# Performance work log

Measured on AMD Instinct MI355X. Metric: run time of the kernel, lower is better.

The kernel has to match this reference:

```python
import jax, jax.numpy as jnp
import numpy as np

DEGREE = 64
LEN_H = 2
INIT_H = 4.0
FEATURES = [256, 512, 512, 256]
BATCH = 1024


def _frozen_kh():
    # get_frozen_para: k = arange(-floor(d/2), ceil(d/2)+1); h = 1/(init_h*(1+arange(len_h))) (inverse decay)
    k = jnp.arange(-np.floor(DEGREE / 2), np.ceil(DEGREE / 2) + 1, dtype=jnp.float32)  # (degree+1,)
    h = 1.0 / (INIT_H * (1.0 + jnp.arange(LEN_H, dtype=jnp.float32)))  # (len_h,)
    return k, h


def setup_inputs() -> dict:
    key = jax.random.key(0)
    ks = jax.random.split(key, 7)
    inp = {"x": jax.random.normal(ks[0], (BATCH, FEATURES[0]), dtype=jnp.float32)}
    i = 1
    for li, (fi, fo) in enumerate(zip(FEATURES[:-1], FEATURES[1:])):
        # initialization='None': plain normal coeffs (matches source)
        inp[f"coeffs{li}"] = jax.random.normal(ks[i], (fi, fo, LEN_H, DEGREE + 1), dtype=jnp.float32)
        inp[f"alpha{li}"] = jax.random.normal(ks[i + 1], (fi, fo), dtype=jnp.float32) / jnp.sqrt((fi + fo) / 2.0)
        inp[f"beta{li}"] = jnp.zeros((fo,), dtype=jnp.float32)
        i += 2
    return inp


def _sinc_layer(x, coeffs, alpha, beta, k, h):
    # x: (b, i); coeffs: (i, o, k_h, d+1); alpha: (i, o); beta: (o,)
    y_eqt = x @ alpha + beta  # skip connection (skip_mode=1)
    xa = jnp.tanh(x)  # activation='tanh'
    # tile across (len_h, degree+1), scale by 1/h, shift by k, then sinc
    xe = xa[:, :, None, None] / h[None, None, :, None] + k[None, None, None, :]  # (b, i, k_h, d+1)
    y = jnp.einsum("bikd,iokd->bo", jnp.sinc(xe), coeffs)
    return y_eqt + y


def reference(x, coeffs0, alpha0, beta0, coeffs1, alpha1, beta1, coeffs2, alpha2, beta2):
    k, h = _frozen_kh()
    x = jnp.tanh(x)  # normalizer
    for c, a, b in ((coeffs0, alpha0, beta0), (coeffs1, alpha1, beta1), (coeffs2, alpha2, beta2)):
        x = _sinc_layer(x, c, a, b, k, h)
    return x
```

## Files before the change

kernel.cpp:

```cpp
#include <hip/hip_runtime.h>
#include <hip/hip_bf16.h>
#include <cstdint>


#define PI_F 3.14159265358979323846f

typedef float floatx4 __attribute__((ext_vector_type(4)));
typedef __bf16 bf16x8 __attribute__((ext_vector_type(8)));

#define GLOAD_LDS16(gp, lp)                                                    \
  __builtin_amdgcn_global_load_lds(                                            \
      (const __attribute__((address_space(1))) void*)(uintptr_t)(const void*)(gp), \
      (__attribute__((address_space(3))) void*)(uint32_t)(uintptr_t)(void*)(lp),   \
      16, 0, 0)

static __device__ __forceinline__ void repack_body(
    const float* __restrict__ coeffs, const float* __restrict__ alpha,
    ushort* __restrict__ Bhi, ushort* __restrict__ Blo,
    int fo, int Kaug, int writeLo, int idx, int tid)
{
  int nchunksK = Kaug >> 8;
  int o     = idx / nchunksK;
  int chunk = idx - o * nchunksK;
  int r = chunk * 256 + tid;
  int i = r / 131;
  int j = r - i * 131;
  float v;
  if (j == 130) {
    v = alpha[(size_t)i * fo + o];
  } else {
    int h1 = (j >= 65) ? 1 : 0;
    int d  = j - (h1 ? 65 : 0);
    v = coeffs[(((size_t)i * fo + o) * 2 + h1) * 65 + d];
  }
  __hip_bfloat16 hb = __float2bfloat16(v);
  Bhi[(size_t)o * Kaug + r] = *(ushort*)&hb;
  if (writeLo) {
    __hip_bfloat16 lb = __float2bfloat16(v - __bfloat162float(hb));
    Blo[(size_t)o * Kaug + r] = *(ushort*)&lb;
  }
}

__global__ __launch_bounds__(256) void repack_all(
    const float* c0, const float* a0, ushort* h0, ushort* l0,
    const float* c1, const float* a1, ushort* h1, ushort* l1,
    const float* c2, const float* a2, ushort* h2,
    int fo0, int fo1, int fo2, int K0, int K1, int K2, int nb0, int nb01)
{
  int b = blockIdx.x, tid = threadIdx.x;
  if (b < nb0)        repack_body(c0, a0, h0, l0, fo0, K0, 1, b,        tid);
  else if (b < nb01)  repack_body(c1, a1, h1, l1, fo1, K1, 1, b - nb0,  tid);
  else                repack_body(c2, a2, h2, 0,  fo2, K2, 0, b - nb01, tid);
}

__global__ __launch_bounds__(256) void repack_kernel(
    const float* __restrict__ coeffs, const float* __restrict__ alpha,
    ushort* __restrict__ Bhi, ushort* __restrict__ Blo,
    int fo, int Kaug, int writeLo)
{
  repack_body(coeffs, alpha, Bhi, Blo, fo, Kaug, writeLo,
              blockIdx.x + blockIdx.y * gridDim.x, threadIdx.x);
}

__global__ __launch_bounds__(256) void act_kernel(
    const float* __restrict__ Xin, ushort* __restrict__ Ahi,
    ushort* __restrict__ Alo, int first, int writeLo)
{
  __shared__ float sm[256][5];
  int tid = threadIdx.x;
  int p0  = blockIdx.x * 256;
  {
    float x  = Xin[p0 + tid];
    float t  = first ? tanhf(x) : x;
    float xa = tanhf(t);
    float z0 = 4.0f * xa, z1 = 8.0f * xa;
    float n0 = rintf(z0), n1 = rintf(z1);
    float s0 = sinf(PI_F * (z0 - n0)) * (1.0f / PI_F);
    float s1 = sinf(PI_F * (z1 - n1)) * (1.0f / PI_F);
    if (((int)n0) & 1) s0 = -s0;
    if (((int)n1) & 1) s1 = -s1;
    sm[tid][0] = t;
    sm[tid][1] = z0;
    sm[tid][2] = s0;
    sm[tid][3] = z1;
    sm[tid][4] = s1;
  }
  __syncthreads();
  size_t base = (size_t)p0 * 131;
  for (int e4 = tid; e4 < 64 * 131; e4 += 256) {
    int f0 = e4 * 4;
    ushort4 hv, lv;
#pragma unroll
    for (int u = 0; u < 4; ++u) {
      int f  = f0 + u;
      int li = f / 131;
      int j  = f - li * 131;
      float t = sm[li][0];
      bool h1 = (j >= 65);
      int d   = h1 ? (j - 65) : j;
      float z = h1 ? sm[li][3] : sm[li][1];
      float s = h1 ? sm[li][4] : sm[li][2];
      int kk  = d - 32;
      float den = z + (float)kk;
      float v = __fdividef(s, den);
      if (kk & 1) v = -v;
      if (den == 0.0f) v = 1.0f;
      if (j == 130)    v = t;
      __hip_bfloat16 hb = __float2bfloat16(v);
      __hip_bfloat16 lb = __float2bfloat16(v - __bfloat162float(hb));
      ((ushort*)&hv)[u] = *(ushort*)&hb;
      ((ushort*)&lv)[u] = *(ushort*)&lb;
    }
    *(ushort4*)(Ahi + base + f0) = hv;
    if (writeLo) *(ushort4*)(Alo + base + f0) = lv;
  }
}

__global__ __launch_bounds__(256, 4) void gemm_bf16_onepass(
    const ushort* __restrict__ Ahi, const ushort* __restrict__ Alo,
    const ushort* __restrict__ Bhi, const ushort* __restrict__ Blo,
    float* __restrict__ Cpart,
    int N, int Kaug, int T, int splitk, int tilesN, int MBN, int nterms)
{
  __shared__ __align__(16) ushort AsH[128 * 32];
  __shared__ __align__(16) ushort AsL[128 * 32];
  __shared__ __align__(16) ushort BsH[128 * 32];
  __shared__ __align__(16) ushort BsL[128 * 32];

  int bx    = blockIdx.x;
  int split = bx % splitk;
  int tile  = bx / splitk;
  int tm = tile / tilesN;
  int tn = tile - tm * tilesN;
  int s0 = (int)(((long long)split * T) / splitk);
  int s1 = (int)(((long long)(split + 1) * T) / splitk);

  int tid  = threadIdx.x;
  int lane = tid & 63;
  int wave = tid >> 6;
  int wm = (wave >> 1) * 64;
  int wn = (wave & 1) * 64;

  floatx4 acc[4][4];
#pragma unroll
  for (int i = 0; i < 4; i++)
#pragma unroll
    for (int j = 0; j < 4; j++) acc[i][j] = floatx4{0.f, 0.f, 0.f, 0.f};

  const ushort* AgH = Ahi + (size_t)tm * 128 * Kaug;
  const ushort* AgL = Alo + (size_t)tm * 128 * Kaug;
  const ushort* BgH = Bhi + (size_t)tn * 128 * Kaug;
  const ushort* BgL = Blo + (size_t)tn * 128 * Kaug;

  int rsub = lane & 15;
  int qc   = lane >> 4;
  int aoff[4], boff[4];
#pragma unroll
  for (int t = 0; t < 4; ++t) {
    int ra = wm + t * 16 + rsub;
    aoff[t] = (ra * 4 + (qc ^ (ra & 3) ^ ((ra >> 2) & 3))) * 8;
    int rb = wn + t * 16 + rsub;
    boff[t] = (rb * 4 + (qc ^ (rb & 3) ^ ((rb >> 2) & 3))) * 8;
  }

  for (int s = s0; s < s1; ++s) {
    int k0 = s * 32;
#pragma unroll
    for (int r = 0; r < 2; ++r) {
      int c   = tid + 256 * r;
      int row = c >> 2;
      int cc  = c & 3;
      int kcg = cc ^ (row & 3) ^ ((row >> 2) & 3);
      size_t goff = (size_t)row * Kaug + k0 + kcg * 8;
      GLOAD_LDS16(AgH + goff, &AsH[c * 8]);
      GLOAD_LDS16(BgH + goff, &BsH[c * 8]);
      if (nterms > 1) {
        GLOAD_LDS16(AgL + goff, &AsL[c * 8]);
        GLOAD_LDS16(BgL + goff, &BsL[c * 8]);
      }
    }
    __syncthreads();

    bf16x8 ah[4], bh[4];
#pragma unroll
    for (int t = 0; t < 4; ++t) ah[t] = *(const bf16x8*)&AsH[aoff[t]];
#pragma unroll
    for (int t = 0; t < 4; ++t) bh[t] = *(const bf16x8*)&BsH[boff[t]];
#pragma unroll
    for (int i = 0; i < 4; ++i)
#pragma unroll
      for (int j = 0; j < 4; ++j)
        acc[i][j] = __builtin_amdgcn_mfma_f32_16x16x32_bf16(
            ah[i], bh[j], acc[i][j], 0, 0, 0);

    if (nterms > 1) {
      bf16x8 bl[4];
#pragma unroll
      for (int t = 0; t < 4; ++t) bl[t] = *(const bf16x8*)&BsL[boff[t]];
#pragma unroll
      for (int i = 0; i < 4; ++i)
#pragma unroll
        for (int j = 0; j < 4; ++j)
          acc[i][j] = __builtin_amdgcn_mfma_f32_16x16x32_bf16(
              ah[i], bl[j], acc[i][j], 0, 0, 0);
      bf16x8 al[4];
#pragma unroll
      for (int t = 0; t < 4; ++t) al[t] = *(const bf16x8*)&AsL[aoff[t]];
#pragma unroll
      for (int i = 0; i < 4; ++i)
#pragma unroll
        for (int j = 0; j < 4; ++j)
          acc[i][j] = __builtin_amdgcn_mfma_f32_16x16x32_bf16(
              al[i], bh[j], acc[i][j], 0, 0, 0);
    }
    __syncthreads();
  }

  float* Cp = Cpart + (size_t)split * MBN;
  int mrow0 = tm * 128 + wm + (lane >> 4) * 4;
  int ncol  = tn * 128 + wn + (lane & 15);
#pragma unroll
  for (int i = 0; i < 4; ++i) {
#pragma unroll
    for (int r = 0; r < 4; ++r) {
      int m = mrow0 + i * 16 + r;
      float* dst = Cp + (size_t)m * N + ncol;
#pragma unroll
      for (int j = 0; j < 4; ++j) dst[j * 16] = acc[i][j][r];
    }
  }
}

__global__ __launch_bounds__(256) void reduce_f32_kernel(
    const float4* __restrict__ Cp, const float* __restrict__ beta,
    float* __restrict__ Xout, int MN4, int N4mask, int splits)
{
  int e = blockIdx.x * 256 + threadIdx.x;
  if (e >= MN4) return;
  float4 sum = Cp[e];
  for (int s = 1; s < splits; ++s) {
    float4 v = Cp[(size_t)s * MN4 + e];
    sum.x += v.x; sum.y += v.y; sum.z += v.z; sum.w += v.w;
  }
  int n0 = (e & N4mask) * 4;
  sum.x += beta[n0]; sum.y += beta[n0 + 1];
  sum.z += beta[n0 + 2]; sum.w += beta[n0 + 3];
  ((float4*)Xout)[e] = sum;
}

extern "C" void kernel_launch(void* const* d_in, const int* in_sizes, int n_in,
                              void* d_out, int out_size, void* d_ws, size_t ws_size,
                              hipStream_t stream)
{
  const float* x = (const float*)d_in[0];
  const float* coeffs[3] = {(const float*)d_in[1], (const float*)d_in[4], (const float*)d_in[7]};
  const float* alpha[3]  = {(const float*)d_in[2], (const float*)d_in[5], (const float*)d_in[8]};
  const float* beta[3]   = {(const float*)d_in[3], (const float*)d_in[6], (const float*)d_in[9]};

  const int fis[3] = {256, 512, 512};
  const int fos[3] = {512, 512, 256};
  const int trm[3] = {3, 3, 1};

  const size_t KMAX = 67072;
  const size_t bsz[3] = {2ull * 512 * 33536 * 2, 2ull * 512 * 67072 * 2,
                         1ull * 256 * 67072 * 2};
  const size_t Ball   = bsz[0] + bsz[1] + bsz[2];
  const size_t B1     = 2ull * 512 * KMAX * 2;
  const size_t needX  = 2ull * 1024 * 512 * 4;

  int MB = 1024, allB = 0;
  size_t cbytes = 67108864;
  for (;;) {
    size_t aB = (size_t)MB * KMAX * 4;
    if (aB + Ball + needX + 67108864 <= ws_size) { allB = 1; cbytes = 67108864; break; }
    if (aB + B1 + needX + 67108864 <= ws_size)   { allB = 0; cbytes = 67108864; break; }
    if (aB + B1 + needX + 33554432 <= ws_size)   { allB = 0; cbytes = 33554432; break; }
    if (MB == 128) { allB = 0; cbytes = 33554432; break; }
    MB >>= 1;
  }
  int nchunks = 1024 / MB;

  char* ws = (char*)d_ws;
  ushort* Ahi = (ushort*)ws;
  ushort* Alo = Ahi + (size_t)MB * KMAX;
  char* Bbase = ws + (size_t)MB * KMAX * 4;
  ushort* Bh[3]; ushort* Bl[3];
  if (allB) {
    char* p = Bbase;
    for (int l = 0; l < 3; ++l) {
      Bh[l] = (ushort*)p;
      Bl[l] = (trm[l] > 1) ? (ushort*)(p + bsz[l] / 2) : (ushort*)p;
      p += bsz[l];
    }
  } else {
    for (int l = 0; l < 3; ++l) {
      Bh[l] = (ushort*)Bbase;
      Bl[l] = (trm[l] > 1) ? (ushort*)(Bbase + B1 / 2) : (ushort*)Bbase;
    }
  }
  size_t bTot = allB ? Ball : B1;
  float* X1    = (float*)(Bbase + bTot);
  float* X2    = X1 + 1024 * 512;
  float* Cpart = X2 + 1024 * 512;

  if (allB) {
    int nb0 = (33536 / 256) * 512;
    int nb1 = (67072 / 256) * 512;
    int nb2 = (67072 / 256) * 256;
    repack_all<<<nb0 + nb1 + nb2, 256, 0, stream>>>(
        coeffs[0], alpha[0], Bh[0], Bl[0],
        coeffs[1], alpha[1], Bh[1], Bl[1],
        coeffs[2], alpha[2], Bh[2],
        fos[0], fos[1], fos[2], 33536, 67072, 67072, nb0, nb0 + nb1);
  }

  const float* Xl = x;
  for (int l = 0; l < 3; ++l) {
    int fi = fis[l], fo = fos[l];
    int Kaug = fi * 131;
    int T = Kaug / 32;
    int tilesN = fo / 128;
    int sk = (int)(cbytes / 4 / ((size_t)MB * fo));
    if (sk < 1) sk = 1;
    int nterms = trm[l];

    if (!allB) {
      repack_kernel<<<dim3(Kaug / 256, fo), 256, 0, stream>>>(
          coeffs[l], alpha[l], Bh[l], Bl[l], fo, Kaug, nterms > 1 ? 1 : 0);
    }

    float* Xout_f = (l == 0) ? X1 : (l == 1 ? X2 : (float*)d_out);
    for (int c = 0; c < nchunks; ++c) {
      int mb0 = c * MB;
      act_kernel<<<(MB * fi) / 256, 256, 0, stream>>>(
          Xl + (size_t)mb0 * fi, Ahi, Alo, l == 0 ? 1 : 0, nterms > 1 ? 1 : 0);
      gemm_bf16_onepass<<<(MB / 128) * tilesN * sk, 256, 0, stream>>>(
          Ahi, (nterms > 1) ? Alo : Ahi, Bh[l], Bl[l],
          Cpart, fo, Kaug, T, sk, tilesN, MB * fo, nterms);
      int MN4 = MB * fo / 4;
      reduce_f32_kernel<<<(MN4 + 255) / 256, 256, 0, stream>>>(
          (const float4*)Cpart, beta[l],
          Xout_f + (size_t)mb0 * fo, MN4, fo / 4 - 1, sk);
    }
    Xl = Xout_f;
  }
}
```

Measured before the change: 1.070 ms.

## Add 256x256-tile 3-term split-bf16 GEMM with double-buffered LDS pipeline

Adds a new GEMM kernel with 512 threads and 256x256 output tiles that computes the hi*hi, hi*lo and lo*hi bf16 product terms. Global-to-LDS loads for the next K step are interleaved between the three MFMA phases using double buffering, explicit vmcnt waits and s_setprio. Split-K is chosen to give about 256 blocks. The larger tile is meant to raise operand reuse and cut LDS and global traffic per flop, in exchange for heavy register pressure (128 accumulator floats per lane) and 128KB of LDS per block. The new kernel is used only when three terms are requested and the shapes divide by 256; otherwise the old kernel runs.

```diff
diff --git a/kernel.cpp b/kernel.cpp
--- a/kernel.cpp
+++ b/kernel.cpp
@@ -13,6 +13,8 @@
       (const __attribute__((address_space(1))) void*)(uintptr_t)(const void*)(gp), \
       (__attribute__((address_space(3))) void*)(uint32_t)(uintptr_t)(void*)(lp),   \
       16, 0, 0)
+
+#define CFENCE() asm volatile("" ::: "memory")
 
 static __device__ __forceinline__ void repack_body(
     const float* __restrict__ coeffs, const float* __restrict__ alpha,
@@ -231,6 +233,173 @@
   }
 }
 
+__global__ __launch_bounds__(512, 2) void gemm256_nt3(
+    const ushort* __restrict__ Ahi, const ushort* __restrict__ Alo,
+    const ushort* __restrict__ Bhi, const ushort* __restrict__ Blo,
+    float* __restrict__ Cpart,
+    int N, int Kaug, int T, int splitk, int tilesN, int MBN)
+{
+  __shared__ __align__(16) ushort AsH[2][8192];
+  __shared__ __align__(16) ushort AsL[2][8192];
+  __shared__ __align__(16) ushort BsH[2][8192];
+  __shared__ __align__(16) ushort BsL[2][8192];
+
+  const int bx    = blockIdx.x;
+  const int split = bx % splitk;
+  const int tile  = bx / splitk;
+  const int tm = tile / tilesN;
+  const int tn = tile - tm * tilesN;
+  const int s0 = (int)(((long long)split * T) / splitk);
+  const int s1 = (int)(((long long)(split + 1) * T) / splitk);
+
+  const int tid  = threadIdx.x;
+  const int lane = tid & 63;
+  const int wave = tid >> 6;
+  const int wm = (wave >> 2) * 128;
+  const int wn = (wave & 3) * 64;
+
+  floatx4 acc[8][4];
+#pragma unroll
+  for (int i = 0; i < 8; ++i)
+#pragma unroll
+    for (int j = 0; j < 4; ++j) acc[i][j] = floatx4{0.f, 0.f, 0.f, 0.f};
+
+  const ushort* AgH = Ahi + (size_t)tm * 256 * Kaug;
+  const ushort* AgL = Alo + (size_t)tm * 256 * Kaug;
+  const ushort* BgH = Bhi + (size_t)tn * 256 * Kaug;
+  const ushort* BgL = Blo + (size_t)tn * 256 * Kaug;
+
+  const int c0 = tid, c1 = tid + 512;
+  const int r0c = c0 >> 2, q0c = c0 & 3;
+  const int r1c = c1 >> 2, q1c = c1 & 3;
+  const size_t g0 = (size_t)r0c * Kaug + (size_t)((q0c ^ (r0c & 3) ^ ((r0c >> 2) & 3)) * 8);
+  const size_t g1 = (size_t)r1c * Kaug + (size_t)((q1c ^ (r1c & 3) ^ ((r1c >> 2) & 3)) * 8);
+  const int d0 = c0 * 8, d1 = c1 * 8;
+
+  const int rsub = lane & 15;
+  const int qc   = lane >> 4;
+  int aoff[8], boff[4];
+#pragma unroll
+  for (int t = 0; t < 8; ++t) {
+    int ra = wm + t * 16 + rsub;
+    aoff[t] = (ra * 4 + (qc ^ (ra & 3) ^ ((ra >> 2) & 3))) * 8;
+  }
+#pragma unroll
+  for (int t = 0; t < 4; ++t) {
+    int rb = wn + t * 16 + rsub;
+    boff[t] = (rb * 4 + (qc ^ (rb & 3) ^ ((rb >> 2) & 3))) * 8;
+  }
+
+  {
+    const int k0 = s0 * 32;
+    GLOAD_LDS16(AgH + g0 + k0, &AsH[0][d0]);
+    GLOAD_LDS16(AgH + g1 + k0, &AsH[0][d1]);
+    GLOAD_LDS16(BgH + g0 + k0, &BsH[0][d0]);
+    GLOAD_LDS16(BgH + g1 + k0, &BsH[0][d1]);
+    GLOAD_LDS16(BgL + g0 + k0, &BsL[0][d0]);
+    GLOAD_LDS16(BgL + g1 + k0, &BsL[0][d1]);
+    GLOAD_LDS16(AgL + g0 + k0, &AsL[0][d0]);
+    GLOAD_LDS16(AgL + g1 + k0, &AsL[0][d1]);
+  }
+  asm volatile("s_waitcnt vmcnt(4)" ::: "memory");
+  __builtin_amdgcn_s_barrier();
+  CFENCE();
+
+  int cur = 0;
+  for (int s = s0; s < s1; ++s) {
+    const int  nxt     = cur ^ 1;
+    const bool notlast = (s + 1 < s1);
+    const int  kn      = (s + 1) * 32;
+
+    bf16x8 ah[8], bh[4];
+#pragma unroll
+    for (int t = 0; t < 8; ++t) ah[t] = *(const bf16x8*)&AsH[cur][aoff[t]];
+#pragma unroll
+    for (int t = 0; t < 4; ++t) bh[t] = *(const bf16x8*)&BsH[cur][boff[t]];
+    if (notlast) {
+      GLOAD_LDS16(AgH + g0 + kn, &AsH[nxt][d0]);
+      GLOAD_LDS16(AgH + g1 + kn, &AsH[nxt][d1]);
+      GLOAD_LDS16(BgH + g0 + kn, &BsH[nxt][d0]);
+      GLOAD_LDS16(BgH + g1 + kn, &BsH[nxt][d1]);
+      asm volatile("s_waitcnt vmcnt(6)" ::: "memory");
+    } else {
+      asm volatile("s_waitcnt vmcnt(2)" ::: "memory");
+    }
+    __builtin_amdgcn_s_barrier();
+    CFENCE();
+    __builtin_amdgcn_s_setprio(1);
+#pragma unroll
+    for (int i = 0; i < 8; ++i)
+#pragma unroll
+      for (int j = 0; j < 4; ++j)
+        acc[i][j] = __builtin_amdgcn_mfma_f32_16x16x32_bf16(
+            ah[i], bh[j], acc[i][j], 0, 0, 0);
+    __builtin_amdgcn_s_setprio(0);
+    __builtin_amdgcn_s_barrier();
+    CFENCE();
+
+    bf16x8 bl[4];
+#pragma unroll
+    for (int t = 0; t < 4; ++t) bl[t] = *(const bf16x8*)&BsL[cur][boff[t]];
+    if (notlast) {
+      GLOAD_LDS16(BgL + g0 + kn, &BsL[nxt][d0]);
+      GLOAD_LDS16(BgL + g1 + kn, &BsL[nxt][d1]);
+      asm volatile("s_waitcnt vmcnt(6)" ::: "memory");
+    } else {
+      asm volatile("s_waitcnt vmcnt(0)" ::: "memory");
+    }
+    __builtin_amdgcn_s_barrier();
+    CFENCE();
+    __builtin_amdgcn_s_setprio(1);
+#pragma unroll
+    for (int i = 0; i < 8; ++i)
+#pragma unroll
+      for (int j = 0; j < 4; ++j)
+        acc[i][j] = __builtin_amdgcn_mfma_f32_16x16x32_bf16(
+            ah[i], bl[j], acc[i][j], 0, 0, 0);
+    __builtin_amdgcn_s_setprio(0);
+    __builtin_amdgcn_s_barrier();
+    CFENCE();
+
+    bf16x8 al[8];
+#pragma unroll
+    for (int t = 0; t < 8; ++t) al[t] = *(const bf16x8*)&AsL[cur][aoff[t]];
+    if (notlast) {
+      GLOAD_LDS16(AgL + g0 + kn, &AsL[nxt][d0]);
+      GLOAD_LDS16(AgL + g1 + kn, &AsL[nxt][d1]);
+      asm volatile("s_waitcnt vmcnt(4)" ::: "memory");
+    }
+    __builtin_amdgcn_s_barrier();
+    CFENCE();
+    __builtin_amdgcn_s_setprio(1);
+#pragma unroll
+    for (int i = 0; i < 8; ++i)
+#pragma unroll
+      for (int j = 0; j < 4; ++j)
+        acc[i][j] = __builtin_amdgcn_mfma_f32_16x16x32_bf16(
+            al[i], bh[j], acc[i][j], 0, 0, 0);
+    __builtin_amdgcn_s_setprio(0);
+    __builtin_amdgcn_s_barrier();
+    CFENCE();
+
+    cur = nxt;
+  }
+
+  float* Cp = Cpart + (size_t)split * MBN;
+  const int mrow0 = tm * 256 + wm + (lane >> 4) * 4;
+  const int ncol  = tn * 256 + wn + (lane & 15);
+#pragma unroll
+  for (int i = 0; i < 8; ++i) {
+#pragma unroll
+    for (int r = 0; r < 4; ++r) {
+      int m = mrow0 + i * 16 + r;
+      float* dst = Cp + (size_t)m * N + ncol;
+#pragma unroll
+      for (int j = 0; j < 4; ++j) dst[j * 16] = acc[i][j][r];
+    }
+  }
+}
+
 __global__ __launch_bounds__(256) void reduce_f32_kernel(
     const float4* __restrict__ Cp, const float* __restrict__ beta,
     float* __restrict__ Xout, int MN4, int N4mask, int splits)
@@ -319,9 +488,6 @@
     int fi = fis[l], fo = fos[l];
     int Kaug = fi * 131;
     int T = Kaug / 32;
-    int tilesN = fo / 128;
-    int sk = (int)(cbytes / 4 / ((size_t)MB * fo));
-    if (sk < 1) sk = 1;
     int nterms = trm[l];
 
     if (!allB) {
@@ -330,17 +496,35 @@
     }
 
     float* Xout_f = (l == 0) ? X1 : (l == 1 ? X2 : (float*)d_out);
+    bool use256 = (nterms > 1) && (MB % 256 == 0) && (fo % 256 == 0);
     for (int c = 0; c < nchunks; ++c) {
       int mb0 = c * MB;
       act_kernel<<<(MB * fi) / 256, 256, 0, stream>>>(
           Xl + (size_t)mb0 * fi, Ahi, Alo, l == 0 ? 1 : 0, nterms > 1 ? 1 : 0);
-      gemm_bf16_onepass<<<(MB / 128) * tilesN * sk, 256, 0, stream>>>(
-          Ahi, (nterms > 1) ? Alo : Ahi, Bh[l], Bl[l],
-          Cpart, fo, Kaug, T, sk, tilesN, MB * fo, nterms);
       int MN4 = MB * fo / 4;
-      reduce_f32_kernel<<<(MN4 + 255) / 256, 256, 0, stream>>>(
-          (const float4*)Cpart, beta[l],
-          Xout_f + (size_t)mb0 * fo, MN4, fo / 4 - 1, sk);
+      if (use256) {
+        int tilesN2 = fo / 256;
+        int tiles2  = (MB / 256) * tilesN2;
+        int skmem   = (int)(cbytes / 4 / ((size_t)MB * fo));
+        int sk2     = 256 / tiles2;
+        if (sk2 > skmem) sk2 = skmem;
+        if (sk2 < 1) sk2 = 1;
+        gemm256_nt3<<<tiles2 * sk2, 512, 0, stream>>>(
+            Ahi, Alo, Bh[l], Bl[l], Cpart, fo, Kaug, T, sk2, tilesN2, MB * fo);
+        reduce_f32_kernel<<<(MN4 + 255) / 256, 256, 0, stream>>>(
+            (const float4*)Cpart, beta[l],
+            Xout_f + (size_t)mb0 * fo, MN4, fo / 4 - 1, sk2);
+      } else {
+        int tilesN = fo / 128;
+        int sk = (int)(cbytes / 4 / ((size_t)MB * fo));
+        if (sk < 1) sk = 1;
+        gemm_bf16_onepass<<<(MB / 128) * tilesN * sk, 256, 0, stream>>>(
+            Ahi, (nterms > 1) ? Alo : Ahi, Bh[l], Bl[l],
+            Cpart, fo, Kaug, T, sk, tilesN, MB * fo, nterms);
+        reduce_f32_kernel<<<(MN4 + 255) / 256, 256, 0, stream>>>(
+            (const float4*)Cpart, beta[l],
+            Xout_f + (size_t)mb0 * fo, MN4, fo / 4 - 1, sk);
+      }
     }
     Xl = Xout_f;
   }
```

Result: faster. 963.1 us (-10.0%).
